# Kernel tuning notes

Hardware: AMD Instinct MI355X
Metric: run time of the kernel (lower is better)

## Reference

```python
import jax, jax.numpy as jnp
import numpy as np
from jax import lax

BS, N, MAXITER = 64, 1024, 50


def setup_inputs() -> dict:
    key = jax.random.key(0)
    kA, kb, kM = jax.random.split(key, 3)
    B = jax.random.normal(kA, (BS, N, N), dtype=jnp.float32)
    # SPD system matrix: A = B B^T / N + I  (well-conditioned for CG)
    A = B @ jnp.swapaxes(B, -1, -2) / N + jnp.eye(N, dtype=jnp.float32)
    b = jax.random.normal(kb, (BS, N, 1), dtype=jnp.float32)
    x0 = jnp.zeros((BS, N, 1), dtype=jnp.float32)
    # learned preconditioner M_inv: positive diagonal (SPD)
    d = 1.0 + jax.random.uniform(kM, (BS, N), dtype=jnp.float32)
    M_inv = jax.vmap(jnp.diag)(d)
    rtol = jnp.zeros((BS,), dtype=jnp.float32)
    return {"A": A, "b": b, "x0": x0, "M_inv": M_inv, "rtol": rtol, "maxiter": MAXITER}


def reference(A, b, x0, M_inv, rtol, maxiter):
    # Batched preconditioned CG. history: (bs, maxiter+1) residual norms.
    def bdot(u, v):  # batched inner product -> (bs,1,1)
        return jnp.sum(u * v, axis=(1, 2), keepdims=True)

    r0 = b - A @ x0                       # (bs,n,1)
    z0 = M_inv @ r0
    rnorm0 = jnp.sqrt(jnp.sum(r0 * r0, axis=(1, 2)))  # (bs,)

    def step(carry, _):
        x, r, z, p = carry
        Ap = A @ p
        rz = bdot(r, z)
        alpha = rz / bdot(p, Ap)
        x = x + alpha * p
        r_new = r - alpha * Ap
        z_new = M_inv @ r_new
        beta = bdot(r_new, z_new) / rz
        p = z_new + beta * p
        rnorm = jnp.sqrt(jnp.sum(r_new * r_new, axis=(1, 2)))
        return (x, r_new, z_new, p), rnorm

    _, hist = lax.scan(step, (x0, r0, z0, z0), None, length=maxiter)
    # hist: (maxiter, bs) -> stack with initial norm -> (bs, maxiter+1)
    return jnp.concatenate([rnorm0[:, None], hist.T], axis=1)
```

## Files before the change

kernel.cpp:

```cpp
#include <hip/hip_runtime.h>
#include <math.h>

#define BS 64
#define N 1024
#define BPB 16
#define JCHUNK (N / BPB)
#define THREADS 256
#define LGRP 16
#define MAXITER 50
#define OUTW (MAXITER + 1)

typedef _Float16 half4 __attribute__((ext_vector_type(4)));
typedef _Float16 half8 __attribute__((ext_vector_type(8)));


__device__ inline float wave_reduce(float v) {
#pragma unroll
    for (int off = 32; off > 0; off >>= 1) v += __shfl_xor(v, off, 64);
    return v;
}

__device__ inline float block_reduce1(float a, float* red, int lane, int wave) {
    a = wave_reduce(a);
    if (lane == 0) red[wave] = a;
    __syncthreads();
    return red[0] + red[1] + red[2] + red[3];
}

__device__ inline float2 block_reduce2(float a, float b, float* redA,
                                       float* redB, int lane, int wave) {
    a = wave_reduce(a);
    b = wave_reduce(b);
    if (lane == 0) {
        redA[wave] = a;
        redB[wave] = b;
    }
    __syncthreads();
    float2 r;
    r.x = redA[0] + redA[1] + redA[2] + redA[3];
    r.y = redB[0] + redB[1] + redB[2] + redB[3];
    return r;
}

__global__ __launch_bounds__(THREADS) void convert_kernel(
    const float* __restrict__ A, _Float16* __restrict__ Ah) {
    const size_t i = ((size_t)blockIdx.x * THREADS + threadIdx.x) * 8;
    const float4* src = (const float4*)(A + i);
    float4 a0 = src[0];
    float4 a1 = src[1];
    half8 h;
    h[0] = (_Float16)a0.x; h[1] = (_Float16)a0.y;
    h[2] = (_Float16)a0.z; h[3] = (_Float16)a0.w;
    h[4] = (_Float16)a1.x; h[5] = (_Float16)a1.y;
    h[6] = (_Float16)a1.z; h[7] = (_Float16)a1.w;
    *(half8*)(Ah + i) = h;
}

__global__ __launch_bounds__(THREADS) void init_p_kernel(
    const float* __restrict__ x0, const float* __restrict__ Minv,
    float* __restrict__ pv, float* __restrict__ dv) {
    const int batch = blockIdx.x;
    const int tid = threadIdx.x;
    const int c0 = 4 * tid;
    ((float4*)(pv + (size_t)batch * N))[tid] =
        ((const float4*)(x0 + (size_t)batch * N))[tid];
    const size_t base = (size_t)batch * N * N;
    float4 dd;
    dd.x = Minv[base + (size_t)(c0 + 0) * (N + 1)];
    dd.y = Minv[base + (size_t)(c0 + 1) * (N + 1)];
    dd.z = Minv[base + (size_t)(c0 + 2) * (N + 1)];
    dd.w = Minv[base + (size_t)(c0 + 3) * (N + 1)];
    ((float4*)(dv + (size_t)batch * N))[tid] = dd;
}

__global__ __launch_bounds__(THREADS, 4) void matvec_kernel(
    const _Float16* __restrict__ Ah, const float* __restrict__ pv,
    float* __restrict__ papv) {
    const int blk = blockIdx.x;
    const int batch = blk / BPB;
    const int chunk = blk % BPB;
    const int j0 = chunk * JCHUNK;
    const int tid = threadIdx.x;

    __shared__ float p_lds[JCHUNK];
    if (tid < JCHUNK) p_lds[tid] = pv[(size_t)batch * N + j0 + tid];
    __syncthreads();

    const half4* __restrict__ A4 =
        (const half4*)(Ah + (size_t)batch * N * N + (size_t)j0 * N);
    float4 acc = {0.f, 0.f, 0.f, 0.f};
#pragma unroll 1
    for (int jb = 0; jb < JCHUNK; jb += LGRP) {
        half4 a[LGRP];
#pragma unroll
        for (int u = 0; u < LGRP; ++u)
            a[u] = A4[(size_t)(jb + u) * (N / 4) + tid];
#pragma unroll
        for (int u = 0; u < LGRP; ++u) {
            float pj = p_lds[jb + u];
            acc.x += (float)a[u][0] * pj;
            acc.y += (float)a[u][1] * pj;
            acc.z += (float)a[u][2] * pj;
            acc.w += (float)a[u][3] * pj;
        }
    }
    ((float4*)(papv + ((size_t)batch * BPB + chunk) * N))[tid] = acc;
}

__global__ __launch_bounds__(THREADS) void init_update_kernel(
    const float* __restrict__ b, const float* __restrict__ papv,
    const float* __restrict__ dv, float* __restrict__ pv,
    float* __restrict__ rv, float* __restrict__ rzs, float* __restrict__ out) {
    const int batch = blockIdx.x;
    const int tid = threadIdx.x;
    const int lane = tid & 63;
    const int wave = tid >> 6;
    __shared__ float redA[4], redB[4];

    const float4* g = (const float4*)(papv + (size_t)batch * BPB * N);
    float4 Ap = {0.f, 0.f, 0.f, 0.f};
#pragma unroll
    for (int c = 0; c < BPB; ++c) {
        float4 t = g[(size_t)c * (N / 4) + tid];
        Ap.x += t.x; Ap.y += t.y; Ap.z += t.z; Ap.w += t.w;
    }
    float4 b4 = ((const float4*)(b + (size_t)batch * N))[tid];
    float4 dd = ((const float4*)(dv + (size_t)batch * N))[tid];
    float4 rr, zz;
    rr.x = b4.x - Ap.x; rr.y = b4.y - Ap.y;
    rr.z = b4.z - Ap.z; rr.w = b4.w - Ap.w;
    zz.x = dd.x * rr.x; zz.y = dd.y * rr.y;
    zz.z = dd.z * rr.z; zz.w = dd.w * rr.w;
    ((float4*)(rv + (size_t)batch * N))[tid] = rr;
    ((float4*)(pv + (size_t)batch * N))[tid] = zz;
    float lrz = rr.x * zz.x + rr.y * zz.y + rr.z * zz.z + rr.w * zz.w;
    float lrn = rr.x * rr.x + rr.y * rr.y + rr.z * rr.z + rr.w * rr.w;
    float2 s = block_reduce2(lrz, lrn, redA, redB, lane, wave);
    if (tid == 0) {
        rzs[batch] = s.x;
        out[batch * OUTW + 0] = sqrtf(s.y);
    }
}

__global__ __launch_bounds__(THREADS) void update_kernel(
    const float* __restrict__ papv, const float* __restrict__ dv,
    float* __restrict__ pv, float* __restrict__ rv, float* __restrict__ rzs,
    float* __restrict__ out, int k) {
    const int batch = blockIdx.x;
    const int tid = threadIdx.x;
    const int lane = tid & 63;
    const int wave = tid >> 6;
    __shared__ float redP[4], redA[4], redB[4];

    const float4* g = (const float4*)(papv + (size_t)batch * BPB * N);
    float4 Ap = {0.f, 0.f, 0.f, 0.f};
#pragma unroll
    for (int c = 0; c < BPB; ++c) {
        float4 t = g[(size_t)c * (N / 4) + tid];
        Ap.x += t.x; Ap.y += t.y; Ap.z += t.z; Ap.w += t.w;
    }
    float4 p4 = ((const float4*)(pv + (size_t)batch * N))[tid];
    float lpap = p4.x * Ap.x + p4.y * Ap.y + p4.z * Ap.z + p4.w * Ap.w;
    float pap = block_reduce1(lpap, redP, lane, wave);
    float rzp = rzs[batch];
    float alpha = rzp / pap;

    float4 rr = ((const float4*)(rv + (size_t)batch * N))[tid];
    float4 dd = ((const float4*)(dv + (size_t)batch * N))[tid];
    rr.x -= alpha * Ap.x; rr.y -= alpha * Ap.y;
    rr.z -= alpha * Ap.z; rr.w -= alpha * Ap.w;
    float4 zz;
    zz.x = dd.x * rr.x; zz.y = dd.y * rr.y;
    zz.z = dd.z * rr.z; zz.w = dd.w * rr.w;
    ((float4*)(rv + (size_t)batch * N))[tid] = rr;

    float lrz = rr.x * zz.x + rr.y * zz.y + rr.z * zz.z + rr.w * zz.w;
    float lrn = rr.x * rr.x + rr.y * rr.y + rr.z * rr.z + rr.w * rr.w;
    float2 s = block_reduce2(lrz, lrn, redA, redB, lane, wave);
    float beta = s.x / rzp;
    float4 pn;
    pn.x = zz.x + beta * p4.x; pn.y = zz.y + beta * p4.y;
    pn.z = zz.z + beta * p4.z; pn.w = zz.w + beta * p4.w;
    ((float4*)(pv + (size_t)batch * N))[tid] = pn;
    if (tid == 0) {
        rzs[batch] = s.x;
        out[batch * OUTW + k] = sqrtf(s.y);
    }
}

extern "C" void kernel_launch(void* const* d_in, const int* in_sizes, int n_in,
                              void* d_out, int out_size, void* d_ws,
                              size_t ws_size, hipStream_t stream) {
    const float* A = (const float*)d_in[0];
    const float* b = (const float*)d_in[1];
    const float* x0 = (const float*)d_in[2];
    const float* Minv = (const float*)d_in[3];
    float* out = (float*)d_out;

    _Float16* Ah = (_Float16*)d_ws;
    float* papv = (float*)(Ah + (size_t)BS * N * N);
    float* rv = papv + (size_t)BS * BPB * N;
    float* pv = rv + (size_t)BS * N;
    float* dv = pv + (size_t)BS * N;
    float* rzs = dv + (size_t)BS * N;

    dim3 blk(THREADS);
    convert_kernel<<<(BS * N * N) / (8 * THREADS), blk, 0, stream>>>(A, Ah);
    init_p_kernel<<<BS, blk, 0, stream>>>(x0, Minv, pv, dv);
    matvec_kernel<<<BS * BPB, blk, 0, stream>>>(Ah, pv, papv);
    init_update_kernel<<<BS, blk, 0, stream>>>(b, papv, dv, pv, rv, rzs, out);
    for (int k = 1; k <= MAXITER; ++k) {
        matvec_kernel<<<BS * BPB, blk, 0, stream>>>(Ah, pv, papv);
        update_kernel<<<BS, blk, 0, stream>>>(papv, dv, pv, rv, rzs, out, k);
    }
}
```

Before: 1.707 ms.

## Fuse CG into one persistent kernel with per-batch atomic barriers

Replaces the per-iteration matvec and update kernel launches with a single persistent kernel of 256 blocks (4 per batch). Blocks synchronise through per-batch atomic counters, and each block redundantly recomputes the full vector update so no p or r vectors go through global memory. The fp16 conversion of A is fused into the initial matvec pass, and double-buffered partial sums avoid races between iterations. Correctness relies on all 256 blocks being co-resident so the spin barrier cannot deadlock, and each block now does more serial matvec work than before.

```diff
diff --git a/kernel.cpp b/kernel.cpp
--- a/kernel.cpp
+++ b/kernel.cpp
@@ -3,15 +3,18 @@
 
 #define BS 64
 #define N 1024
-#define BPB 16
+#define BPB 4
 #define JCHUNK (N / BPB)
+#define SPB 4
+#define NSLOT 16
 #define THREADS 256
 #define LGRP 16
 #define MAXITER 50
 #define OUTW (MAXITER + 1)
+#define CNT_STRIDE 16
+#define SPIN_MAX (1 << 22)
 
 typedef _Float16 half4 __attribute__((ext_vector_type(4)));
-typedef _Float16 half8 __attribute__((ext_vector_type(8)));
 
 
 __device__ inline float wave_reduce(float v) {
@@ -42,155 +45,183 @@
     return r;
 }
 
-__global__ __launch_bounds__(THREADS) void convert_kernel(
-    const float* __restrict__ A, _Float16* __restrict__ Ah) {
-    const size_t i = ((size_t)blockIdx.x * THREADS + threadIdx.x) * 8;
-    const float4* src = (const float4*)(A + i);
-    float4 a0 = src[0];
-    float4 a1 = src[1];
-    half8 h;
-    h[0] = (_Float16)a0.x; h[1] = (_Float16)a0.y;
-    h[2] = (_Float16)a0.z; h[3] = (_Float16)a0.w;
-    h[4] = (_Float16)a1.x; h[5] = (_Float16)a1.y;
-    h[6] = (_Float16)a1.z; h[7] = (_Float16)a1.w;
-    *(half8*)(Ah + i) = h;
-}
-
-__global__ __launch_bounds__(THREADS) void init_p_kernel(
+__global__ void zero_cnt_kernel(int* __restrict__ cnt) {
+    if (threadIdx.x < BS) cnt[threadIdx.x * CNT_STRIDE] = 0;
+}
+
+__device__ inline void batch_barrier(int* mycnt, int target, int tid) {
+    __threadfence();
+    __syncthreads();
+    if (tid == 0) {
+        __hip_atomic_fetch_add(mycnt, 1, __ATOMIC_RELEASE,
+                               __HIP_MEMORY_SCOPE_AGENT);
+        int spins = 0;
+        while (__hip_atomic_load(mycnt, __ATOMIC_ACQUIRE,
+                                 __HIP_MEMORY_SCOPE_AGENT) < target &&
+               spins < SPIN_MAX) {
+            __builtin_amdgcn_s_sleep(2);
+            ++spins;
+        }
+    }
+    __syncthreads();
+    __threadfence();
+}
+
+__global__ __launch_bounds__(THREADS, 2) void cg_persistent(
+    const float* __restrict__ A, const float* __restrict__ bvec,
     const float* __restrict__ x0, const float* __restrict__ Minv,
-    float* __restrict__ pv, float* __restrict__ dv) {
-    const int batch = blockIdx.x;
-    const int tid = threadIdx.x;
-    const int c0 = 4 * tid;
-    ((float4*)(pv + (size_t)batch * N))[tid] =
-        ((const float4*)(x0 + (size_t)batch * N))[tid];
-    const size_t base = (size_t)batch * N * N;
-    float4 dd;
-    dd.x = Minv[base + (size_t)(c0 + 0) * (N + 1)];
-    dd.y = Minv[base + (size_t)(c0 + 1) * (N + 1)];
-    dd.z = Minv[base + (size_t)(c0 + 2) * (N + 1)];
-    dd.w = Minv[base + (size_t)(c0 + 3) * (N + 1)];
-    ((float4*)(dv + (size_t)batch * N))[tid] = dd;
-}
-
-__global__ __launch_bounds__(THREADS, 4) void matvec_kernel(
-    const _Float16* __restrict__ Ah, const float* __restrict__ pv,
-    float* __restrict__ papv) {
+    _Float16* __restrict__ Ah, float* __restrict__ papv,
+    int* __restrict__ cnt, float* __restrict__ out) {
     const int blk = blockIdx.x;
     const int batch = blk / BPB;
     const int chunk = blk % BPB;
     const int j0 = chunk * JCHUNK;
     const int tid = threadIdx.x;
-
-    __shared__ float p_lds[JCHUNK];
-    if (tid < JCHUNK) p_lds[tid] = pv[(size_t)batch * N + j0 + tid];
-    __syncthreads();
-
-    const half4* __restrict__ A4 =
-        (const half4*)(Ah + (size_t)batch * N * N + (size_t)j0 * N);
-    float4 acc = {0.f, 0.f, 0.f, 0.f};
-#pragma unroll 1
-    for (int jb = 0; jb < JCHUNK; jb += LGRP) {
-        half4 a[LGRP];
-#pragma unroll
-        for (int u = 0; u < LGRP; ++u)
-            a[u] = A4[(size_t)(jb + u) * (N / 4) + tid];
-#pragma unroll
-        for (int u = 0; u < LGRP; ++u) {
-            float pj = p_lds[jb + u];
-            acc.x += (float)a[u][0] * pj;
-            acc.y += (float)a[u][1] * pj;
-            acc.z += (float)a[u][2] * pj;
-            acc.w += (float)a[u][3] * pj;
-        }
-    }
-    ((float4*)(papv + ((size_t)batch * BPB + chunk) * N))[tid] = acc;
-}
-
-__global__ __launch_bounds__(THREADS) void init_update_kernel(
-    const float* __restrict__ b, const float* __restrict__ papv,
-    const float* __restrict__ dv, float* __restrict__ pv,
-    float* __restrict__ rv, float* __restrict__ rzs, float* __restrict__ out) {
-    const int batch = blockIdx.x;
-    const int tid = threadIdx.x;
     const int lane = tid & 63;
     const int wave = tid >> 6;
-    __shared__ float redA[4], redB[4];
-
-    const float4* g = (const float4*)(papv + (size_t)batch * BPB * N);
+
+    __shared__ float p_lds[JCHUNK];
+    __shared__ float redP[4], redA[4], redB[4];
+
+    int* mycnt = cnt + batch * CNT_STRIDE;
+    const size_t mbase = (size_t)batch * N * N;
+
+    const int c0 = 4 * tid;
+    float4 dd;
+    dd.x = Minv[mbase + (size_t)(c0 + 0) * (N + 1)];
+    dd.y = Minv[mbase + (size_t)(c0 + 1) * (N + 1)];
+    dd.z = Minv[mbase + (size_t)(c0 + 2) * (N + 1)];
+    dd.w = Minv[mbase + (size_t)(c0 + 3) * (N + 1)];
+
+    p_lds[tid] = x0[(size_t)batch * N + j0 + tid];
+    __syncthreads();
+
+    const float* Arow = A + mbase + (size_t)j0 * N;
+    _Float16* Hrow = Ah + mbase + (size_t)j0 * N;
+    float4 acc0 = {0.f, 0.f, 0.f, 0.f};
+    float4 acc1 = {0.f, 0.f, 0.f, 0.f};
+    float4 acc2 = {0.f, 0.f, 0.f, 0.f};
+    float4 acc3 = {0.f, 0.f, 0.f, 0.f};
+#pragma unroll
+    for (int sb = 0; sb < SPB; ++sb) {
+#pragma unroll 4
+        for (int rr_ = 0; rr_ < 64; ++rr_) {
+            const int r = sb * 64 + rr_;
+            float4 av = ((const float4*)(Arow + (size_t)r * N))[tid];
+            half4 h;
+            h[0] = (_Float16)av.x; h[1] = (_Float16)av.y;
+            h[2] = (_Float16)av.z; h[3] = (_Float16)av.w;
+            ((half4*)(Hrow + (size_t)r * N))[tid] = h;
+            float pj = p_lds[r];
+            float4* acc = (sb == 0) ? &acc0 : (sb == 1) ? &acc1
+                        : (sb == 2) ? &acc2 : &acc3;
+            acc->x += (float)h[0] * pj; acc->y += (float)h[1] * pj;
+            acc->z += (float)h[2] * pj; acc->w += (float)h[3] * pj;
+        }
+    }
+    {
+        float* papw = papv + ((size_t)batch * NSLOT + SPB * chunk) * N;
+        ((float4*)papw)[tid] = acc0;
+        ((float4*)(papw + N))[tid] = acc1;
+        ((float4*)(papw + 2 * N))[tid] = acc2;
+        ((float4*)(papw + 3 * N))[tid] = acc3;
+    }
+    batch_barrier(mycnt, BPB, tid);
+
+    const float4* g0 = (const float4*)(papv + (size_t)batch * NSLOT * N);
     float4 Ap = {0.f, 0.f, 0.f, 0.f};
 #pragma unroll
-    for (int c = 0; c < BPB; ++c) {
-        float4 t = g[(size_t)c * (N / 4) + tid];
+    for (int c = 0; c < NSLOT; ++c) {
+        float4 t = g0[(size_t)c * (N / 4) + tid];
         Ap.x += t.x; Ap.y += t.y; Ap.z += t.z; Ap.w += t.w;
     }
-    float4 b4 = ((const float4*)(b + (size_t)batch * N))[tid];
-    float4 dd = ((const float4*)(dv + (size_t)batch * N))[tid];
-    float4 rr, zz;
+    float4 b4 = ((const float4*)(bvec + (size_t)batch * N))[tid];
+    float4 rr, pp;
     rr.x = b4.x - Ap.x; rr.y = b4.y - Ap.y;
     rr.z = b4.z - Ap.z; rr.w = b4.w - Ap.w;
-    zz.x = dd.x * rr.x; zz.y = dd.y * rr.y;
-    zz.z = dd.z * rr.z; zz.w = dd.w * rr.w;
-    ((float4*)(rv + (size_t)batch * N))[tid] = rr;
-    ((float4*)(pv + (size_t)batch * N))[tid] = zz;
-    float lrz = rr.x * zz.x + rr.y * zz.y + rr.z * zz.z + rr.w * zz.w;
+    pp.x = dd.x * rr.x; pp.y = dd.y * rr.y;
+    pp.z = dd.z * rr.z; pp.w = dd.w * rr.w;
+    float lrz = rr.x * pp.x + rr.y * pp.y + rr.z * pp.z + rr.w * pp.w;
     float lrn = rr.x * rr.x + rr.y * rr.y + rr.z * rr.z + rr.w * rr.w;
     float2 s = block_reduce2(lrz, lrn, redA, redB, lane, wave);
-    if (tid == 0) {
-        rzs[batch] = s.x;
-        out[batch * OUTW + 0] = sqrtf(s.y);
-    }
-}
-
-__global__ __launch_bounds__(THREADS) void update_kernel(
-    const float* __restrict__ papv, const float* __restrict__ dv,
-    float* __restrict__ pv, float* __restrict__ rv, float* __restrict__ rzs,
-    float* __restrict__ out, int k) {
-    const int batch = blockIdx.x;
-    const int tid = threadIdx.x;
-    const int lane = tid & 63;
-    const int wave = tid >> 6;
-    __shared__ float redP[4], redA[4], redB[4];
-
-    const float4* g = (const float4*)(papv + (size_t)batch * BPB * N);
-    float4 Ap = {0.f, 0.f, 0.f, 0.f};
-#pragma unroll
-    for (int c = 0; c < BPB; ++c) {
-        float4 t = g[(size_t)c * (N / 4) + tid];
-        Ap.x += t.x; Ap.y += t.y; Ap.z += t.z; Ap.w += t.w;
-    }
-    float4 p4 = ((const float4*)(pv + (size_t)batch * N))[tid];
-    float lpap = p4.x * Ap.x + p4.y * Ap.y + p4.z * Ap.z + p4.w * Ap.w;
-    float pap = block_reduce1(lpap, redP, lane, wave);
-    float rzp = rzs[batch];
-    float alpha = rzp / pap;
-
-    float4 rr = ((const float4*)(rv + (size_t)batch * N))[tid];
-    float4 dd = ((const float4*)(dv + (size_t)batch * N))[tid];
-    rr.x -= alpha * Ap.x; rr.y -= alpha * Ap.y;
-    rr.z -= alpha * Ap.z; rr.w -= alpha * Ap.w;
-    float4 zz;
-    zz.x = dd.x * rr.x; zz.y = dd.y * rr.y;
-    zz.z = dd.z * rr.z; zz.w = dd.w * rr.w;
-    ((float4*)(rv + (size_t)batch * N))[tid] = rr;
-
-    float lrz = rr.x * zz.x + rr.y * zz.y + rr.z * zz.z + rr.w * zz.w;
-    float lrn = rr.x * rr.x + rr.y * rr.y + rr.z * rr.z + rr.w * rr.w;
-    float2 s = block_reduce2(lrz, lrn, redA, redB, lane, wave);
-    float beta = s.x / rzp;
-    float4 pn;
-    pn.x = zz.x + beta * p4.x; pn.y = zz.y + beta * p4.y;
-    pn.z = zz.z + beta * p4.z; pn.w = zz.w + beta * p4.w;
-    ((float4*)(pv + (size_t)batch * N))[tid] = pn;
-    if (tid == 0) {
-        rzs[batch] = s.x;
-        out[batch * OUTW + k] = sqrtf(s.y);
+    float rz = s.x;
+    if (chunk == 0 && tid == 0) out[batch * OUTW + 0] = sqrtf(s.y);
+
+    const half4* A4 = (const half4*)(Ah + mbase + (size_t)j0 * N);
+    const int tlo = j0 >> 2;
+    for (int k = 1; k <= MAXITER; ++k) {
+        const int par = k & 1;
+        __syncthreads();
+        if (tid >= tlo && tid < tlo + JCHUNK / 4)
+            ((float4*)p_lds)[tid - tlo] = pp;
+        __syncthreads();
+
+        float4 aA0 = {0.f, 0.f, 0.f, 0.f};
+        float4 aA1 = {0.f, 0.f, 0.f, 0.f};
+        float4 aA2 = {0.f, 0.f, 0.f, 0.f};
+        float4 aA3 = {0.f, 0.f, 0.f, 0.f};
+#pragma unroll
+        for (int sb = 0; sb < SPB; ++sb) {
+            float4* acc = (sb == 0) ? &aA0 : (sb == 1) ? &aA1
+                        : (sb == 2) ? &aA2 : &aA3;
+#pragma unroll 1
+            for (int jb = sb * 64; jb < sb * 64 + 64; jb += LGRP) {
+                half4 a[LGRP];
+#pragma unroll
+                for (int u = 0; u < LGRP; ++u)
+                    a[u] = A4[(size_t)(jb + u) * (N / 4) + tid];
+#pragma unroll
+                for (int u = 0; u < LGRP; ++u) {
+                    float pj = p_lds[jb + u];
+                    acc->x += (float)a[u][0] * pj;
+                    acc->y += (float)a[u][1] * pj;
+                    acc->z += (float)a[u][2] * pj;
+                    acc->w += (float)a[u][3] * pj;
+                }
+            }
+        }
+        {
+            float* papw =
+                papv + (((size_t)par * BS + batch) * NSLOT + SPB * chunk) * N;
+            ((float4*)papw)[tid] = aA0;
+            ((float4*)(papw + N))[tid] = aA1;
+            ((float4*)(papw + 2 * N))[tid] = aA2;
+            ((float4*)(papw + 3 * N))[tid] = aA3;
+        }
+        batch_barrier(mycnt, BPB * (k + 1), tid);
+
+        const float4* gr =
+            (const float4*)(papv + ((size_t)par * BS + batch) * NSLOT * N);
+        float4 Apn = {0.f, 0.f, 0.f, 0.f};
+#pragma unroll
+        for (int c = 0; c < NSLOT; ++c) {
+            float4 t = gr[(size_t)c * (N / 4) + tid];
+            Apn.x += t.x; Apn.y += t.y; Apn.z += t.z; Apn.w += t.w;
+        }
+        float lpap =
+            pp.x * Apn.x + pp.y * Apn.y + pp.z * Apn.z + pp.w * Apn.w;
+        float pap = block_reduce1(lpap, redP, lane, wave);
+        float alpha = rz / pap;
+        rr.x -= alpha * Apn.x; rr.y -= alpha * Apn.y;
+        rr.z -= alpha * Apn.z; rr.w -= alpha * Apn.w;
+        float4 zz;
+        zz.x = dd.x * rr.x; zz.y = dd.y * rr.y;
+        zz.z = dd.z * rr.z; zz.w = dd.w * rr.w;
+        float lrz2 = rr.x * zz.x + rr.y * zz.y + rr.z * zz.z + rr.w * zz.w;
+        float lrn2 = rr.x * rr.x + rr.y * rr.y + rr.z * rr.z + rr.w * rr.w;
+        float2 s2 = block_reduce2(lrz2, lrn2, redA, redB, lane, wave);
+        float beta = s2.x / rz;
+        rz = s2.x;
+        pp.x = zz.x + beta * pp.x; pp.y = zz.y + beta * pp.y;
+        pp.z = zz.z + beta * pp.z; pp.w = zz.w + beta * pp.w;
+        if (chunk == 0 && tid == 0) out[batch * OUTW + k] = sqrtf(s2.y);
     }
 }
 
 extern "C" void kernel_launch(void* const* d_in, const int* in_sizes, int n_in,
                               void* d_out, int out_size, void* d_ws,
                               size_t ws_size, hipStream_t stream) {
+    (void)in_sizes; (void)n_in; (void)out_size; (void)ws_size;
     const float* A = (const float*)d_in[0];
     const float* b = (const float*)d_in[1];
     const float* x0 = (const float*)d_in[2];
@@ -199,18 +230,9 @@
 
     _Float16* Ah = (_Float16*)d_ws;
     float* papv = (float*)(Ah + (size_t)BS * N * N);
-    float* rv = papv + (size_t)BS * BPB * N;
-    float* pv = rv + (size_t)BS * N;
-    float* dv = pv + (size_t)BS * N;
-    float* rzs = dv + (size_t)BS * N;
-
-    dim3 blk(THREADS);
-    convert_kernel<<<(BS * N * N) / (8 * THREADS), blk, 0, stream>>>(A, Ah);
-    init_p_kernel<<<BS, blk, 0, stream>>>(x0, Minv, pv, dv);
-    matvec_kernel<<<BS * BPB, blk, 0, stream>>>(Ah, pv, papv);
-    init_update_kernel<<<BS, blk, 0, stream>>>(b, papv, dv, pv, rv, rzs, out);
-    for (int k = 1; k <= MAXITER; ++k) {
-        matvec_kernel<<<BS * BPB, blk, 0, stream>>>(Ah, pv, papv);
-        update_kernel<<<BS, blk, 0, stream>>>(papv, dv, pv, rv, rzs, out, k);
-    }
-}
+    int* cnt = (int*)(papv + (size_t)2 * BS * NSLOT * N);
+
+    zero_cnt_kernel<<<1, 64, 0, stream>>>(cnt);
+    cg_persistent<<<BS * BPB, THREADS, 0, stream>>>(A, b, x0, Minv, Ah, papv,
+                                                    cnt, out);
+}
```

After: 5.169 ms. 3.03x slower.

## Exploit symmetry of A to read only upper-triangular bands in matvec

Applied to the files above, without the earlier changes.

Replaces the column-chunked matvec with a banded kernel that reads only the block upper triangle of the symmetric fp16 matrix. Each loaded band row contributes both to A·p (column use) and, via a wave reduction, to the transposed product for earlier entries. The update kernels reassemble Ap from the two partial buffers. This aims to roughly halve matrix bandwidth per iteration, at the cost of many cross-lane reductions and load imbalance across bands.

```diff
diff --git a/kernel.cpp b/kernel.cpp
--- a/kernel.cpp
+++ b/kernel.cpp
@@ -3,8 +3,8 @@
 
 #define BS 64
 #define N 1024
-#define BPB 16
-#define JCHUNK (N / BPB)
+#define NBAND 16
+#define BROWS 64
 #define THREADS 256
 #define LGRP 16
 #define MAXITER 50
@@ -73,57 +73,91 @@
     ((float4*)(dv + (size_t)batch * N))[tid] = dd;
 }
 
-__global__ __launch_bounds__(THREADS, 4) void matvec_kernel(
+__global__ __launch_bounds__(THREADS, 4) void tmv_kernel(
     const _Float16* __restrict__ Ah, const float* __restrict__ pv,
-    float* __restrict__ papv) {
+    float* __restrict__ papc1, float* __restrict__ papc2) {
     const int blk = blockIdx.x;
-    const int batch = blk / BPB;
-    const int chunk = blk % BPB;
-    const int j0 = chunk * JCHUNK;
-    const int tid = threadIdx.x;
-
-    __shared__ float p_lds[JCHUNK];
-    if (tid < JCHUNK) p_lds[tid] = pv[(size_t)batch * N + j0 + tid];
-    __syncthreads();
+    const int batch = blk / NBAND;
+    const int band = blk % NBAND;
+    const int tid = threadIdx.x;
+    const int lane = tid & 63;
+    const int wave = tid >> 6;
+
+    __shared__ float p_band[BROWS];
+    __shared__ float rowdot[BROWS][4];
+
+    if (tid < BROWS)
+        p_band[tid] = pv[(size_t)batch * N + (size_t)band * BROWS + tid];
+    __syncthreads();
+
+    const bool act1 = tid < 16 * (band + 1);
+    const bool act2 = tid < 16 * band;
+    const float4 pc = ((const float4*)(pv + (size_t)batch * N))[tid];
 
     const half4* __restrict__ A4 =
-        (const half4*)(Ah + (size_t)batch * N * N + (size_t)j0 * N);
+        (const half4*)(Ah + (size_t)batch * N * N + (size_t)band * BROWS * N);
     float4 acc = {0.f, 0.f, 0.f, 0.f};
 #pragma unroll 1
-    for (int jb = 0; jb < JCHUNK; jb += LGRP) {
+    for (int jb = 0; jb < BROWS; jb += LGRP) {
         half4 a[LGRP];
 #pragma unroll
-        for (int u = 0; u < LGRP; ++u)
-            a[u] = A4[(size_t)(jb + u) * (N / 4) + tid];
-#pragma unroll
         for (int u = 0; u < LGRP; ++u) {
-            float pj = p_lds[jb + u];
-            acc.x += (float)a[u][0] * pj;
-            acc.y += (float)a[u][1] * pj;
-            acc.z += (float)a[u][2] * pj;
-            acc.w += (float)a[u][3] * pj;
+            half4 av = {};
+            if (act1) av = A4[(size_t)(jb + u) * (N / 4) + tid];
+            a[u] = av;
         }
-    }
-    ((float4*)(papv + ((size_t)batch * BPB + chunk) * N))[tid] = acc;
+#pragma unroll
+        for (int u = 0; u < LGRP; ++u) {
+            const float a0 = (float)a[u][0], a1 = (float)a[u][1];
+            const float a2 = (float)a[u][2], a3 = (float)a[u][3];
+            const float pj = p_band[jb + u];
+            acc.x += a0 * pj; acc.y += a1 * pj;
+            acc.z += a2 * pj; acc.w += a3 * pj;
+            float s = 0.f;
+            if (act2) s = a0 * pc.x + a1 * pc.y + a2 * pc.z + a3 * pc.w;
+            s = wave_reduce(s);
+            if (lane == 0) rowdot[jb + u][wave] = s;
+        }
+    }
+    if (act1)
+        ((float4*)(papc1 + ((size_t)batch * NBAND + band) * N))[tid] = acc;
+    __syncthreads();
+    if (tid < BROWS)
+        papc2[((size_t)batch * NBAND + band) * BROWS + tid] =
+            rowdot[tid][0] + rowdot[tid][1] + rowdot[tid][2] + rowdot[tid][3];
+}
+
+__device__ inline float4 assemble_Ap(const float* __restrict__ papc1,
+                                     const float* __restrict__ papc2,
+                                     int batch, int tid) {
+    const int g = tid >> 4;
+    float4 Ap = {0.f, 0.f, 0.f, 0.f};
+#pragma unroll
+    for (int bnd = 0; bnd < NBAND; ++bnd) {
+        if (bnd >= g) {
+            float4 v =
+                ((const float4*)(papc1 + ((size_t)batch * NBAND + bnd) * N))[tid];
+            Ap.x += v.x; Ap.y += v.y; Ap.z += v.z; Ap.w += v.w;
+        }
+    }
+    float4 c2 =
+        ((const float4*)(papc2 + ((size_t)batch * NBAND + g) * BROWS))[tid & 15];
+    Ap.x += c2.x; Ap.y += c2.y; Ap.z += c2.z; Ap.w += c2.w;
+    return Ap;
 }
 
 __global__ __launch_bounds__(THREADS) void init_update_kernel(
-    const float* __restrict__ b, const float* __restrict__ papv,
-    const float* __restrict__ dv, float* __restrict__ pv,
-    float* __restrict__ rv, float* __restrict__ rzs, float* __restrict__ out) {
+    const float* __restrict__ b, const float* __restrict__ papc1,
+    const float* __restrict__ papc2, const float* __restrict__ dv,
+    float* __restrict__ pv, float* __restrict__ rv, float* __restrict__ rzs,
+    float* __restrict__ out) {
     const int batch = blockIdx.x;
     const int tid = threadIdx.x;
     const int lane = tid & 63;
     const int wave = tid >> 6;
     __shared__ float redA[4], redB[4];
 
-    const float4* g = (const float4*)(papv + (size_t)batch * BPB * N);
-    float4 Ap = {0.f, 0.f, 0.f, 0.f};
-#pragma unroll
-    for (int c = 0; c < BPB; ++c) {
-        float4 t = g[(size_t)c * (N / 4) + tid];
-        Ap.x += t.x; Ap.y += t.y; Ap.z += t.z; Ap.w += t.w;
-    }
+    float4 Ap = assemble_Ap(papc1, papc2, batch, tid);
     float4 b4 = ((const float4*)(b + (size_t)batch * N))[tid];
     float4 dd = ((const float4*)(dv + (size_t)batch * N))[tid];
     float4 rr, zz;
@@ -143,22 +177,17 @@
 }
 
 __global__ __launch_bounds__(THREADS) void update_kernel(
-    const float* __restrict__ papv, const float* __restrict__ dv,
-    float* __restrict__ pv, float* __restrict__ rv, float* __restrict__ rzs,
-    float* __restrict__ out, int k) {
+    const float* __restrict__ papc1, const float* __restrict__ papc2,
+    const float* __restrict__ dv, float* __restrict__ pv,
+    float* __restrict__ rv, float* __restrict__ rzs, float* __restrict__ out,
+    int k) {
     const int batch = blockIdx.x;
     const int tid = threadIdx.x;
     const int lane = tid & 63;
     const int wave = tid >> 6;
     __shared__ float redP[4], redA[4], redB[4];
 
-    const float4* g = (const float4*)(papv + (size_t)batch * BPB * N);
-    float4 Ap = {0.f, 0.f, 0.f, 0.f};
-#pragma unroll
-    for (int c = 0; c < BPB; ++c) {
-        float4 t = g[(size_t)c * (N / 4) + tid];
-        Ap.x += t.x; Ap.y += t.y; Ap.z += t.z; Ap.w += t.w;
-    }
+    float4 Ap = assemble_Ap(papc1, papc2, batch, tid);
     float4 p4 = ((const float4*)(pv + (size_t)batch * N))[tid];
     float lpap = p4.x * Ap.x + p4.y * Ap.y + p4.z * Ap.z + p4.w * Ap.w;
     float pap = block_reduce1(lpap, redP, lane, wave);
@@ -191,6 +220,7 @@
 extern "C" void kernel_launch(void* const* d_in, const int* in_sizes, int n_in,
                               void* d_out, int out_size, void* d_ws,
                               size_t ws_size, hipStream_t stream) {
+    (void)in_sizes; (void)n_in; (void)out_size; (void)ws_size;
     const float* A = (const float*)d_in[0];
     const float* b = (const float*)d_in[1];
     const float* x0 = (const float*)d_in[2];
@@ -198,8 +228,9 @@
     float* out = (float*)d_out;
 
     _Float16* Ah = (_Float16*)d_ws;
-    float* papv = (float*)(Ah + (size_t)BS * N * N);
-    float* rv = papv + (size_t)BS * BPB * N;
+    float* papc1 = (float*)(Ah + (size_t)BS * N * N);
+    float* papc2 = papc1 + (size_t)BS * NBAND * N;
+    float* rv = papc2 + (size_t)BS * NBAND * BROWS;
     float* pv = rv + (size_t)BS * N;
     float* dv = pv + (size_t)BS * N;
     float* rzs = dv + (size_t)BS * N;
@@ -207,10 +238,12 @@
     dim3 blk(THREADS);
     convert_kernel<<<(BS * N * N) / (8 * THREADS), blk, 0, stream>>>(A, Ah);
     init_p_kernel<<<BS, blk, 0, stream>>>(x0, Minv, pv, dv);
-    matvec_kernel<<<BS * BPB, blk, 0, stream>>>(Ah, pv, papv);
-    init_update_kernel<<<BS, blk, 0, stream>>>(b, papv, dv, pv, rv, rzs, out);
+    tmv_kernel<<<BS * NBAND, blk, 0, stream>>>(Ah, pv, papc1, papc2);
+    init_update_kernel<<<BS, blk, 0, stream>>>(b, papc1, papc2, dv, pv, rv,
+                                               rzs, out);
     for (int k = 1; k <= MAXITER; ++k) {
-        matvec_kernel<<<BS * BPB, blk, 0, stream>>>(Ah, pv, papv);
-        update_kernel<<<BS, blk, 0, stream>>>(papv, dv, pv, rv, rzs, out, k);
-    }
-}
+        tmv_kernel<<<BS * NBAND, blk, 0, stream>>>(Ah, pv, papc1, papc2);
+        update_kernel<<<BS, blk, 0, stream>>>(papc1, papc2, dv, pv, rv, rzs,
+                                              out, k);
+    }
+}
```

After: 2.155 ms. 26.3% more time.

## Fuse CG vector update into column-panel matvec and merge conversion with first matvec

Applied to the files above, without the earlier changes.

Each matvec block now recomputes the per-batch CG update (alpha, r, z, beta, p) redundantly from the previous full A·p vector, then computes a 64-column panel of A·p using A's symmetry, so the separate update kernel and the 16-way partial-sum buffer are gone. It uses ping-pong buffers for r, p, y and rz. The fp32-to-fp16 conversion is fused with the initial matvec, and a small final kernel handles the last residual. This halves kernel launches and removes the partial-product traffic, at the cost of redundant per-block reductions across 16 chunks.

```diff
diff --git a/kernel.cpp b/kernel.cpp
--- a/kernel.cpp
+++ b/kernel.cpp
@@ -3,15 +3,14 @@
 
 #define BS 64
 #define N 1024
-#define BPB 16
-#define JCHUNK (N / BPB)
+#define NCHUNK 16
+#define CCOLS 64
 #define THREADS 256
-#define LGRP 16
+#define LGRP 8
 #define MAXITER 50
 #define OUTW (MAXITER + 1)
 
 typedef _Float16 half4 __attribute__((ext_vector_type(4)));
-typedef _Float16 half8 __attribute__((ext_vector_type(8)));
 
 
 __device__ inline float wave_reduce(float v) {
@@ -42,155 +41,186 @@
     return r;
 }
 
-__global__ __launch_bounds__(THREADS) void convert_kernel(
-    const float* __restrict__ A, _Float16* __restrict__ Ah) {
-    const size_t i = ((size_t)blockIdx.x * THREADS + threadIdx.x) * 8;
-    const float4* src = (const float4*)(A + i);
-    float4 a0 = src[0];
-    float4 a1 = src[1];
-    half8 h;
-    h[0] = (_Float16)a0.x; h[1] = (_Float16)a0.y;
-    h[2] = (_Float16)a0.z; h[3] = (_Float16)a0.w;
-    h[4] = (_Float16)a1.x; h[5] = (_Float16)a1.y;
-    h[6] = (_Float16)a1.z; h[7] = (_Float16)a1.w;
-    *(half8*)(Ah + i) = h;
-}
-
-__global__ __launch_bounds__(THREADS) void init_p_kernel(
-    const float* __restrict__ x0, const float* __restrict__ Minv,
-    float* __restrict__ pv, float* __restrict__ dv) {
-    const int batch = blockIdx.x;
+__device__ inline void panel_store(float4 acc, float* wredf, float* ydst,
+                                   int tid) {
+    acc.x += __shfl_xor(acc.x, 16, 64); acc.x += __shfl_xor(acc.x, 32, 64);
+    acc.y += __shfl_xor(acc.y, 16, 64); acc.y += __shfl_xor(acc.y, 32, 64);
+    acc.z += __shfl_xor(acc.z, 16, 64); acc.z += __shfl_xor(acc.z, 32, 64);
+    acc.w += __shfl_xor(acc.w, 16, 64); acc.w += __shfl_xor(acc.w, 32, 64);
+    const int lane = tid & 63;
+    const int wave = tid >> 6;
+    if (lane < 16) {
+        float* w4 = wredf + wave * 64 + lane * 4;
+        w4[0] = acc.x; w4[1] = acc.y; w4[2] = acc.z; w4[3] = acc.w;
+    }
+    __syncthreads();
+    if (tid < CCOLS)
+        ydst[tid] =
+            wredf[tid] + wredf[64 + tid] + wredf[128 + tid] + wredf[192 + tid];
+}
+
+__global__ __launch_bounds__(THREADS, 4) void l0_kernel(
+    const float* __restrict__ A, const float* __restrict__ x0,
+    const float* __restrict__ Minv, _Float16* __restrict__ Ah,
+    float* __restrict__ yv, float* __restrict__ dv) {
+    const int batch = blockIdx.x >> 4;
+    const int chunk = blockIdx.x & 15;
+    const int c0 = chunk * CCOLS;
     const int tid = threadIdx.x;
-    const int c0 = 4 * tid;
-    ((float4*)(pv + (size_t)batch * N))[tid] =
-        ((const float4*)(x0 + (size_t)batch * N))[tid];
-    const size_t base = (size_t)batch * N * N;
-    float4 dd;
-    dd.x = Minv[base + (size_t)(c0 + 0) * (N + 1)];
-    dd.y = Minv[base + (size_t)(c0 + 1) * (N + 1)];
-    dd.z = Minv[base + (size_t)(c0 + 2) * (N + 1)];
-    dd.w = Minv[base + (size_t)(c0 + 3) * (N + 1)];
-    ((float4*)(dv + (size_t)batch * N))[tid] = dd;
-}
-
-__global__ __launch_bounds__(THREADS, 4) void matvec_kernel(
-    const _Float16* __restrict__ Ah, const float* __restrict__ pv,
-    float* __restrict__ papv) {
-    const int blk = blockIdx.x;
-    const int batch = blk / BPB;
-    const int chunk = blk % BPB;
-    const int j0 = chunk * JCHUNK;
-    const int tid = threadIdx.x;
-
-    __shared__ float p_lds[JCHUNK];
-    if (tid < JCHUNK) p_lds[tid] = pv[(size_t)batch * N + j0 + tid];
-    __syncthreads();
-
-    const half4* __restrict__ A4 =
-        (const half4*)(Ah + (size_t)batch * N * N + (size_t)j0 * N);
+
+    __shared__ float p_lds[N];
+    __shared__ float wredf[256];
+
+    const size_t vb = (size_t)batch * N;
+    ((float4*)p_lds)[tid] = ((const float4*)(x0 + vb))[tid];
+    if (tid < CCOLS)
+        dv[vb + c0 + tid] =
+            Minv[(size_t)batch * N * N + (size_t)(c0 + tid) * (N + 1)];
+    __syncthreads();
+
+    const int rg = tid >> 4;
+    const int cq4 = (c0 >> 2) + (tid & 15);
+    const float4* __restrict__ Af = (const float4*)(A + (size_t)batch * N * N);
+    half4* __restrict__ Ah4 = (half4*)(Ah + (size_t)batch * N * N);
     float4 acc = {0.f, 0.f, 0.f, 0.f};
 #pragma unroll 1
-    for (int jb = 0; jb < JCHUNK; jb += LGRP) {
+    for (int sb = 0; sb < 64; sb += LGRP) {
+        float4 av[LGRP];
+#pragma unroll
+        for (int u = 0; u < LGRP; ++u)
+            av[u] = Af[(size_t)(rg + 16 * (sb + u)) * (N / 4) + cq4];
+#pragma unroll
+        for (int u = 0; u < LGRP; ++u) {
+            half4 h;
+            h[0] = (_Float16)av[u].x; h[1] = (_Float16)av[u].y;
+            h[2] = (_Float16)av[u].z; h[3] = (_Float16)av[u].w;
+            Ah4[(size_t)(rg + 16 * (sb + u)) * (N / 4) + cq4] = h;
+            const float pj = p_lds[rg + 16 * (sb + u)];
+            acc.x += (float)h[0] * pj; acc.y += (float)h[1] * pj;
+            acc.z += (float)h[2] * pj; acc.w += (float)h[3] * pj;
+        }
+    }
+    panel_store(acc, wredf, yv + vb + c0, tid);
+}
+
+__global__ __launch_bounds__(THREADS, 4) void iter_kernel(
+    const _Float16* __restrict__ Ah, const float* __restrict__ bvec,
+    const float* __restrict__ dv, float* __restrict__ yv,
+    float* __restrict__ rv2, float* __restrict__ pv2,
+    float* __restrict__ rzs2, float* __restrict__ out, int k) {
+    const int batch = blockIdx.x >> 4;
+    const int chunk = blockIdx.x & 15;
+    const int c0 = chunk * CCOLS;
+    const int tid = threadIdx.x;
+    const int lane = tid & 63;
+    const int wave = tid >> 6;
+
+    __shared__ float p_lds[N];
+    __shared__ float wredf[256];
+    __shared__ float redP[4], redA[4], redB[4];
+
+    const int ro = (k - 1) & 1;
+    const int wo = k & 1;
+    const size_t vb = (size_t)batch * N;
+    const size_t vro = (size_t)ro * BS * N + vb;
+    const size_t vwo = (size_t)wo * BS * N + vb;
+
+    float4 y4 = ((const float4*)(yv + vro))[tid];
+    float4 dd = ((const float4*)(dv + vb))[tid];
+    float4 rr, pp;
+    float rz_new, rn;
+    if (k == 1) {
+        float4 b4 = ((const float4*)(bvec + vb))[tid];
+        rr.x = b4.x - y4.x; rr.y = b4.y - y4.y;
+        rr.z = b4.z - y4.z; rr.w = b4.w - y4.w;
+        pp.x = dd.x * rr.x; pp.y = dd.y * rr.y;
+        pp.z = dd.z * rr.z; pp.w = dd.w * rr.w;
+        float lrz = rr.x * pp.x + rr.y * pp.y + rr.z * pp.z + rr.w * pp.w;
+        float lrn = rr.x * rr.x + rr.y * rr.y + rr.z * rr.z + rr.w * rr.w;
+        float2 s = block_reduce2(lrz, lrn, redA, redB, lane, wave);
+        rz_new = s.x; rn = s.y;
+    } else {
+        float4 p4 = ((const float4*)(pv2 + vro))[tid];
+        rr = ((const float4*)(rv2 + vro))[tid];
+        const float rzp = rzs2[ro * BS + batch];
+        float lpap = p4.x * y4.x + p4.y * y4.y + p4.z * y4.z + p4.w * y4.w;
+        float pap = block_reduce1(lpap, redP, lane, wave);
+        float alpha = rzp / pap;
+        rr.x -= alpha * y4.x; rr.y -= alpha * y4.y;
+        rr.z -= alpha * y4.z; rr.w -= alpha * y4.w;
+        float4 zz;
+        zz.x = dd.x * rr.x; zz.y = dd.y * rr.y;
+        zz.z = dd.z * rr.z; zz.w = dd.w * rr.w;
+        float lrz = rr.x * zz.x + rr.y * zz.y + rr.z * zz.z + rr.w * zz.w;
+        float lrn = rr.x * rr.x + rr.y * rr.y + rr.z * rr.z + rr.w * rr.w;
+        float2 s = block_reduce2(lrz, lrn, redA, redB, lane, wave);
+        rz_new = s.x; rn = s.y;
+        float beta = rz_new / rzp;
+        pp.x = zz.x + beta * p4.x; pp.y = zz.y + beta * p4.y;
+        pp.z = zz.z + beta * p4.z; pp.w = zz.w + beta * p4.w;
+    }
+    if (chunk == 0) {
+        ((float4*)(rv2 + vwo))[tid] = rr;
+        ((float4*)(pv2 + vwo))[tid] = pp;
+        if (tid == 0) {
+            rzs2[wo * BS + batch] = rz_new;
+            out[batch * OUTW + (k - 1)] = sqrtf(rn);
+        }
+    }
+    ((float4*)p_lds)[tid] = pp;
+    __syncthreads();
+
+    const int rg = tid >> 4;
+    const int cq4 = (c0 >> 2) + (tid & 15);
+    const half4* __restrict__ A4 = (const half4*)(Ah + (size_t)batch * N * N);
+    float4 acc = {0.f, 0.f, 0.f, 0.f};
+#pragma unroll 1
+    for (int sb = 0; sb < 64; sb += LGRP) {
         half4 a[LGRP];
 #pragma unroll
         for (int u = 0; u < LGRP; ++u)
-            a[u] = A4[(size_t)(jb + u) * (N / 4) + tid];
+            a[u] = A4[(size_t)(rg + 16 * (sb + u)) * (N / 4) + cq4];
 #pragma unroll
         for (int u = 0; u < LGRP; ++u) {
-            float pj = p_lds[jb + u];
+            const float pj = p_lds[rg + 16 * (sb + u)];
             acc.x += (float)a[u][0] * pj;
             acc.y += (float)a[u][1] * pj;
             acc.z += (float)a[u][2] * pj;
             acc.w += (float)a[u][3] * pj;
         }
     }
-    ((float4*)(papv + ((size_t)batch * BPB + chunk) * N))[tid] = acc;
-}
-
-__global__ __launch_bounds__(THREADS) void init_update_kernel(
-    const float* __restrict__ b, const float* __restrict__ papv,
-    const float* __restrict__ dv, float* __restrict__ pv,
-    float* __restrict__ rv, float* __restrict__ rzs, float* __restrict__ out) {
+    panel_store(acc, wredf, yv + vwo + c0, tid);
+}
+
+__global__ __launch_bounds__(THREADS) void final_kernel(
+    const float* __restrict__ yv, const float* __restrict__ pv2,
+    const float* __restrict__ rv2, const float* __restrict__ rzs2,
+    float* __restrict__ out) {
     const int batch = blockIdx.x;
     const int tid = threadIdx.x;
     const int lane = tid & 63;
     const int wave = tid >> 6;
-    __shared__ float redA[4], redB[4];
-
-    const float4* g = (const float4*)(papv + (size_t)batch * BPB * N);
-    float4 Ap = {0.f, 0.f, 0.f, 0.f};
-#pragma unroll
-    for (int c = 0; c < BPB; ++c) {
-        float4 t = g[(size_t)c * (N / 4) + tid];
-        Ap.x += t.x; Ap.y += t.y; Ap.z += t.z; Ap.w += t.w;
-    }
-    float4 b4 = ((const float4*)(b + (size_t)batch * N))[tid];
-    float4 dd = ((const float4*)(dv + (size_t)batch * N))[tid];
-    float4 rr, zz;
-    rr.x = b4.x - Ap.x; rr.y = b4.y - Ap.y;
-    rr.z = b4.z - Ap.z; rr.w = b4.w - Ap.w;
-    zz.x = dd.x * rr.x; zz.y = dd.y * rr.y;
-    zz.z = dd.z * rr.z; zz.w = dd.w * rr.w;
-    ((float4*)(rv + (size_t)batch * N))[tid] = rr;
-    ((float4*)(pv + (size_t)batch * N))[tid] = zz;
-    float lrz = rr.x * zz.x + rr.y * zz.y + rr.z * zz.z + rr.w * zz.w;
+    __shared__ float redP[4], redA[4];
+
+    const size_t vb = (size_t)batch * N;
+    float4 y4 = ((const float4*)(yv + vb))[tid];
+    float4 p4 = ((const float4*)(pv2 + vb))[tid];
+    float4 rr = ((const float4*)(rv2 + vb))[tid];
+    const float rzp = rzs2[batch];
+    float lpap = p4.x * y4.x + p4.y * y4.y + p4.z * y4.z + p4.w * y4.w;
+    float pap = block_reduce1(lpap, redP, lane, wave);
+    float alpha = rzp / pap;
+    rr.x -= alpha * y4.x; rr.y -= alpha * y4.y;
+    rr.z -= alpha * y4.z; rr.w -= alpha * y4.w;
     float lrn = rr.x * rr.x + rr.y * rr.y + rr.z * rr.z + rr.w * rr.w;
-    float2 s = block_reduce2(lrz, lrn, redA, redB, lane, wave);
-    if (tid == 0) {
-        rzs[batch] = s.x;
-        out[batch * OUTW + 0] = sqrtf(s.y);
-    }
-}
-
-__global__ __launch_bounds__(THREADS) void update_kernel(
-    const float* __restrict__ papv, const float* __restrict__ dv,
-    float* __restrict__ pv, float* __restrict__ rv, float* __restrict__ rzs,
-    float* __restrict__ out, int k) {
-    const int batch = blockIdx.x;
-    const int tid = threadIdx.x;
-    const int lane = tid & 63;
-    const int wave = tid >> 6;
-    __shared__ float redP[4], redA[4], redB[4];
-
-    const float4* g = (const float4*)(papv + (size_t)batch * BPB * N);
-    float4 Ap = {0.f, 0.f, 0.f, 0.f};
-#pragma unroll
-    for (int c = 0; c < BPB; ++c) {
-        float4 t = g[(size_t)c * (N / 4) + tid];
-        Ap.x += t.x; Ap.y += t.y; Ap.z += t.z; Ap.w += t.w;
-    }
-    float4 p4 = ((const float4*)(pv + (size_t)batch * N))[tid];
-    float lpap = p4.x * Ap.x + p4.y * Ap.y + p4.z * Ap.z + p4.w * Ap.w;
-    float pap = block_reduce1(lpap, redP, lane, wave);
-    float rzp = rzs[batch];
-    float alpha = rzp / pap;
-
-    float4 rr = ((const float4*)(rv + (size_t)batch * N))[tid];
-    float4 dd = ((const float4*)(dv + (size_t)batch * N))[tid];
-    rr.x -= alpha * Ap.x; rr.y -= alpha * Ap.y;
-    rr.z -= alpha * Ap.z; rr.w -= alpha * Ap.w;
-    float4 zz;
-    zz.x = dd.x * rr.x; zz.y = dd.y * rr.y;
-    zz.z = dd.z * rr.z; zz.w = dd.w * rr.w;
-    ((float4*)(rv + (size_t)batch * N))[tid] = rr;
-
-    float lrz = rr.x * zz.x + rr.y * zz.y + rr.z * zz.z + rr.w * zz.w;
-    float lrn = rr.x * rr.x + rr.y * rr.y + rr.z * rr.z + rr.w * rr.w;
-    float2 s = block_reduce2(lrz, lrn, redA, redB, lane, wave);
-    float beta = s.x / rzp;
-    float4 pn;
-    pn.x = zz.x + beta * p4.x; pn.y = zz.y + beta * p4.y;
-    pn.z = zz.z + beta * p4.z; pn.w = zz.w + beta * p4.w;
-    ((float4*)(pv + (size_t)batch * N))[tid] = pn;
-    if (tid == 0) {
-        rzs[batch] = s.x;
-        out[batch * OUTW + k] = sqrtf(s.y);
-    }
+    float rn = block_reduce1(lrn, redA, lane, wave);
+    if (tid == 0) out[batch * OUTW + MAXITER] = sqrtf(rn);
 }
 
 extern "C" void kernel_launch(void* const* d_in, const int* in_sizes, int n_in,
                               void* d_out, int out_size, void* d_ws,
                               size_t ws_size, hipStream_t stream) {
+    (void)in_sizes; (void)n_in; (void)out_size; (void)ws_size;
     const float* A = (const float*)d_in[0];
     const float* b = (const float*)d_in[1];
     const float* x0 = (const float*)d_in[2];
@@ -198,19 +228,16 @@
     float* out = (float*)d_out;
 
     _Float16* Ah = (_Float16*)d_ws;
-    float* papv = (float*)(Ah + (size_t)BS * N * N);
-    float* rv = papv + (size_t)BS * BPB * N;
-    float* pv = rv + (size_t)BS * N;
-    float* dv = pv + (size_t)BS * N;
-    float* rzs = dv + (size_t)BS * N;
+    float* yv = (float*)(Ah + (size_t)BS * N * N);
+    float* rv2 = yv + (size_t)2 * BS * N;
+    float* pv2 = rv2 + (size_t)2 * BS * N;
+    float* dv = pv2 + (size_t)2 * BS * N;
+    float* rzs2 = dv + (size_t)BS * N;
 
     dim3 blk(THREADS);
-    convert_kernel<<<(BS * N * N) / (8 * THREADS), blk, 0, stream>>>(A, Ah);
-    init_p_kernel<<<BS, blk, 0, stream>>>(x0, Minv, pv, dv);
-    matvec_kernel<<<BS * BPB, blk, 0, stream>>>(Ah, pv, papv);
-    init_update_kernel<<<BS, blk, 0, stream>>>(b, papv, dv, pv, rv, rzs, out);
-    for (int k = 1; k <= MAXITER; ++k) {
-        matvec_kernel<<<BS * BPB, blk, 0, stream>>>(Ah, pv, papv);
-        update_kernel<<<BS, blk, 0, stream>>>(papv, dv, pv, rv, rzs, out, k);
-    }
-}
+    l0_kernel<<<BS * NCHUNK, blk, 0, stream>>>(A, x0, Minv, Ah, yv, dv);
+    for (int k = 1; k <= MAXITER; ++k)
+        iter_kernel<<<BS * NCHUNK, blk, 0, stream>>>(Ah, b, dv, yv, rv2, pv2,
+                                                     rzs2, out, k);
+    final_kernel<<<BS, blk, 0, stream>>>(yv, pv2, rv2, rzs2, out);
+}
```

Result: faster. 1.565 ms (-8.3%).
